# Kernel tuning notes

Measured on AMD Instinct MI355X. Metric: run time of the kernel, lower is better.

The kernel has to match this reference:

```python
import jax, jax.numpy as jnp
import numpy as np


def setup_inputs() -> dict:
    key = jax.random.key(0)
    ks = jax.random.split(key, 7)
    B, I, H, O, T = 1024, 2048, 2048, 2048, 30
    s = 1.0 / np.sqrt(H)
    return {
        "x": jax.random.normal(ks[0], (B, I), dtype=jnp.float32),
        "w_ih": jax.random.uniform(ks[1], (3 * H, I), jnp.float32, -s, s),
        "w_hh": jax.random.uniform(ks[2], (3 * H, H), jnp.float32, -s, s),
        "b_ih": jax.random.uniform(ks[3], (3 * H,), jnp.float32, -s, s),
        "b_hh": jax.random.uniform(ks[4], (3 * H,), jnp.float32, -s, s),
        "w_cls": jax.random.uniform(ks[5], (O, H), jnp.float32, -s, s),
        "b_cls": jax.random.uniform(ks[6], (O,), jnp.float32, -s, s),
        "num_timesteps": T,
    }


def reference(x, w_ih, w_hh, b_ih, b_hh, w_cls, b_cls, num_timesteps):
    # Original module never updates hidden_unit inside the loop, so every
    # timestep computes GRUCell(x, 0) -> identical output. Compute once,
    # broadcast across T (same math as the torch loop).
    # GRUCell with h=0: W_hh @ h vanishes; only bias_hh contributes.
    gi = x @ w_ih.T + b_ih                      # [B, 3H]
    i_r, i_z, i_n = jnp.split(gi, 3, axis=1)    # each [B, H]
    h_r, h_z, h_n = jnp.split(b_hh, 3)          # each [H]
    r = jax.nn.sigmoid(i_r + h_r)
    z = jax.nn.sigmoid(i_z + h_z)
    n = jnp.tanh(i_n + r * h_n)
    h_new = (1.0 - z) * n                       # + z * 0
    out = jax.nn.sigmoid(h_new @ w_cls.T + b_cls)  # [B, O]
    B, O = out.shape
    # torch stacks along dim 2 -> [B, O, T]; squeeze is a no-op for B,O,T > 1
    return jnp.broadcast_to(out[:, :, None], (B, O, num_timesteps))
```

## Files before the change

kernel.cpp:

```cpp
#include <hip/hip_runtime.h>
#include <hip/hip_bf16.h>
#include <math.h>

typedef __attribute__((ext_vector_type(8))) _Float16 f16x8;
typedef __attribute__((ext_vector_type(4))) float f32x4;

static __device__ __forceinline__ float sigmoidf_(float x) {
    return 1.0f / (1.0f + expf(-x));
}

__global__ void cvt_all(const float* __restrict__ s0, _Float16* __restrict__ d0, int n0,
                        const float* __restrict__ s1, _Float16* __restrict__ d1, int n1,
                        const float* __restrict__ s2, _Float16* __restrict__ d2, int n2,
                        int ck01, int ck2)
{
    int c = blockIdx.x * 256 + threadIdx.x;
    const float* s; _Float16* d; int ck;
    if (c < n0)            { s = s0; d = d0; ck = ck01; }
    else if (c < n0 + n1)  { c -= n0; s = s1; d = d1; ck = ck01; }
    else                   { c -= n0 + n1; if (c >= n2) return; s = s2; d = d2; ck = ck2; }
    const int row = c / ck;
    const int kc  = c - row * ck;
    const int kcs = (kc & ~7) | ((kc & 7) ^ (row & 7));
    const float* sp = s + (size_t)c * 8;
    float4 v0 = *(const float4*)sp;
    float4 v1 = *(const float4*)(sp + 4);
    f16x8 h;
    h[0] = (_Float16)v0.x; h[1] = (_Float16)v0.y;
    h[2] = (_Float16)v0.z; h[3] = (_Float16)v0.w;
    h[4] = (_Float16)v1.x; h[5] = (_Float16)v1.y;
    h[6] = (_Float16)v1.z; h[7] = (_Float16)v1.w;
    *(f16x8*)(d + (size_t)row * ((size_t)ck * 8) + (size_t)kcs * 8) = h;
}

template <int BM, int BN, int EPI>
__launch_bounds__(256, 2)
__global__ void gemm_mw(const _Float16* __restrict__ A, const _Float16* __restrict__ Bw,
                        const float* __restrict__ bias, void* __restrict__ Cv,
                        int N, int K)
{
    constexpr int BK = 64;
    constexpr int WM = BM / 2, WN = BN / 2;
    constexpr int MR = WM / 16, NR = WN / 16;

    __shared__ _Float16 As[BM * BK];
    __shared__ _Float16 Bs[BN * BK];

    const int tid  = threadIdx.x;
    const int lane = tid & 63;
    const int wid  = tid >> 6;
    const int wr   = wid >> 1;
    const int wc   = wid & 1;
    const int brow = blockIdx.y * BM;
    const int bcol = blockIdx.x * BN;
    const int lr   = lane & 15;
    const int kb   = lane >> 4;

    const _Float16* ap = A  + (size_t)(brow + (tid >> 3)) * K + (tid & 7) * 8;
    const _Float16* bp = Bw + (size_t)(bcol + (tid >> 3)) * K + (tid & 7) * 8;

    f32x4 acc[MR][NR] = {};

    for (int k0 = 0; k0 < K; k0 += BK) {
        __syncthreads();
#pragma unroll
        for (int c0 = 0; c0 < BM * 8; c0 += 256)
            __builtin_amdgcn_global_load_lds(
                (const __attribute__((address_space(1))) void*)(ap + k0 + (size_t)(c0 >> 3) * K),
                (__attribute__((address_space(3))) void*)&As[(c0 + tid) * 8],
                16, 0, 0);
#pragma unroll
        for (int c0 = 0; c0 < BN * 8; c0 += 256)
            __builtin_amdgcn_global_load_lds(
                (const __attribute__((address_space(1))) void*)(bp + k0 + (size_t)(c0 >> 3) * K),
                (__attribute__((address_space(3))) void*)&Bs[(c0 + tid) * 8],
                16, 0, 0);
        __syncthreads();

#pragma unroll
        for (int ks = 0; ks < 2; ++ks) {
            f16x8 af[MR], bf[NR];
#pragma unroll
            for (int m = 0; m < MR; ++m) {
                const int row = wr * WM + m * 16 + lr;
                af[m] = *(const f16x8*)&As[row * BK + ((ks * 4 + kb) ^ (row & 7)) * 8];
            }
#pragma unroll
            for (int n = 0; n < NR; ++n) {
                const int row = wc * WN + n * 16 + lr;
                bf[n] = *(const f16x8*)&Bs[row * BK + ((ks * 4 + kb) ^ (row & 7)) * 8];
            }
#pragma unroll
            for (int n = 0; n < NR; ++n)
#pragma unroll
                for (int m = 0; m < MR; ++m)
                    acc[m][n] = __builtin_amdgcn_mfma_f32_16x16x32_f16(af[m], bf[n], acc[m][n], 0, 0, 0);
        }
    }

#pragma unroll
    for (int m = 0; m < MR; ++m) {
        const int r0 = brow + wr * WM + m * 16 + kb * 4;
#pragma unroll
        for (int n = 0; n < NR; ++n) {
            const int col = bcol + wc * WN + n * 16 + lr;
            const float bv = bias[col];
#pragma unroll
            for (int j = 0; j < 4; ++j) {
                const float v = acc[m][n][j] + bv;
                if (EPI == 0)
                    ((_Float16*)Cv)[(size_t)(r0 + j) * N + col] = (_Float16)v;
                else
                    ((float*)Cv)[(size_t)(r0 + j) * N + col] = sigmoidf_(v);
            }
        }
    }
}

__global__ void gate_swz(const _Float16* __restrict__ gi, const float* __restrict__ b_hh,
                         _Float16* __restrict__ hn, int B, int H)
{
    const int ch = H >> 3;
    const int c = blockIdx.x * 256 + threadIdx.x;
    if (c >= B * ch) return;
    const int b  = c / ch;
    const int hc = c - b * ch;
    const int h0 = hc * 8;
    const _Float16* g = gi + (size_t)b * 3 * H + h0;
    f16x8 ir = *(const f16x8*)g;
    f16x8 iz = *(const f16x8*)(g + H);
    f16x8 in = *(const f16x8*)(g + 2 * H);
    float hr[8], hz[8], hnn[8];
    *(float4*)&hr[0]  = *(const float4*)(b_hh + h0);
    *(float4*)&hr[4]  = *(const float4*)(b_hh + h0 + 4);
    *(float4*)&hz[0]  = *(const float4*)(b_hh + H + h0);
    *(float4*)&hz[4]  = *(const float4*)(b_hh + H + h0 + 4);
    *(float4*)&hnn[0] = *(const float4*)(b_hh + 2 * H + h0);
    *(float4*)&hnn[4] = *(const float4*)(b_hh + 2 * H + h0 + 4);
    f16x8 o;
#pragma unroll
    for (int q = 0; q < 8; ++q) {
        const float r = sigmoidf_((float)ir[q] + hr[q]);
        const float z = sigmoidf_((float)iz[q] + hz[q]);
        o[q] = (_Float16)((1.0f - z) * tanhf((float)in[q] + r * hnn[q]));
    }
    const int hcs = (hc & ~7) | ((hc & 7) ^ (b & 7));
    *(f16x8*)(hn + (size_t)b * H + (size_t)hcs * 8) = o;
}

__global__ void bcast_kernel(const float* __restrict__ res,
                             float* __restrict__ out, int BO, int T)
{
    const int bo0 = blockIdx.x * 256;
    if (T & 1) {
        float* op = out + (size_t)bo0 * T;
        const int n = 256 * T;
        for (int j = threadIdx.x; j < n; j += blockDim.x)
            op[j] = res[bo0 + j / T];
    } else {
        const int half = T >> 1;
        float2* o2 = (float2*)(out + (size_t)bo0 * T);
        const int n2 = 256 * half;
        for (int j = threadIdx.x; j < n2; j += blockDim.x) {
            const float v = res[bo0 + j / half];
            o2[j] = make_float2(v, v);
        }
    }
}

extern "C" void kernel_launch(void* const* d_in, const int* in_sizes, int n_in,
                              void* d_out, int out_size, void* d_ws, size_t ws_size,
                              hipStream_t stream)
{
    const float* x     = (const float*)d_in[0];
    const float* w_ih  = (const float*)d_in[1];
    const float* b_ih  = (const float*)d_in[3];
    const float* b_hh  = (const float*)d_in[4];
    const float* w_cls = (const float*)d_in[5];
    const float* b_cls = (const float*)d_in[6];

    const int H3 = in_sizes[3];
    const int H  = H3 / 3;
    const int I  = in_sizes[1] / H3;
    const int B  = in_sizes[0] / I;
    const int O  = in_sizes[6];
    const int T  = out_size / (B * O);

    _Float16* x16    = (_Float16*)d_ws;
    _Float16* wcls16 = x16 + (size_t)B * I;
    _Float16* hn16   = wcls16 + (size_t)O * H;
    float*    res    = (float*)(hn16 + (size_t)B * H);

    _Float16* wih16 = (_Float16*)d_out;
    _Float16* gi16  = wih16 + (size_t)H3 * I;

    dim3 blk(256);

    {
        const int n0 = B * I / 8, n1 = H3 * I / 8, n2 = O * H / 8;
        const int tot = n0 + n1 + n2;
        cvt_all<<<(tot + 255) / 256, blk, 0, stream>>>(x, x16, n0, w_ih, wih16, n1,
                                                       w_cls, wcls16, n2, I / 8, H / 8);
    }

    gemm_mw<128, 96, 0><<<dim3(H3 / 96, B / 128), blk, 0, stream>>>(
        x16, wih16, b_ih, gi16, H3, I);

    gate_swz<<<(B * H / 8 + 255) / 256, blk, 0, stream>>>(gi16, b_hh, hn16, B, H);

    gemm_mw<64, 64, 1><<<dim3(O / 64, B / 64), blk, 0, stream>>>(
        hn16, wcls16, b_cls, res, O, H);

    bcast_kernel<<<(B * O) / 256, blk, 0, stream>>>(res, (float*)d_out, B * O, T);
}
```

Before: 411.0 us.

## Fuse GRU gate into first GEMM and broadcast into classifier GEMM with double buffering

The first GEMM now tiles over the three gate slices of one hidden range, so the r/z/n gate math runs in its epilogue and the f16 gi intermediate plus the separate gate kernel go away. The classifier GEMM stages sigmoid outputs in shared memory and writes the T-fold broadcast output directly, removing the res buffer and the broadcast kernel. Both GEMMs switch to double-buffered LDS with global_load_lds prefetch of the next K tile, at the cost of more shared memory per block and possibly lower occupancy. The broadcast write pattern from each block is less contiguous than the old flat broadcast kernel.

```diff
diff --git a/kernel.cpp b/kernel.cpp
--- a/kernel.cpp
+++ b/kernel.cpp
@@ -8,6 +8,10 @@
 static __device__ __forceinline__ float sigmoidf_(float x) {
     return 1.0f / (1.0f + expf(-x));
 }
+
+#define GLL(src, dst) __builtin_amdgcn_global_load_lds(                         \
+        (const __attribute__((address_space(1))) void*)(src),                   \
+        (__attribute__((address_space(3))) void*)(dst), 16, 0, 0)
 
 __global__ void cvt_all(const float* __restrict__ s0, _Float16* __restrict__ d0, int n0,
                         const float* __restrict__ s1, _Float16* __restrict__ d1, int n1,
@@ -33,62 +37,166 @@
     *(f16x8*)(d + (size_t)row * ((size_t)ck * 8) + (size_t)kcs * 8) = h;
 }
 
-template <int BM, int BN, int EPI>
 __launch_bounds__(256, 2)
-__global__ void gemm_mw(const _Float16* __restrict__ A, const _Float16* __restrict__ Bw,
-                        const float* __restrict__ bias, void* __restrict__ Cv,
-                        int N, int K)
-{
-    constexpr int BK = 64;
-    constexpr int WM = BM / 2, WN = BN / 2;
-    constexpr int MR = WM / 16, NR = WN / 16;
-
-    __shared__ _Float16 As[BM * BK];
-    __shared__ _Float16 Bs[BN * BK];
+__global__ void gemm1_gate(const _Float16* __restrict__ A,
+                           const _Float16* __restrict__ W,
+                           const float* __restrict__ b_ih,
+                           const float* __restrict__ b_hh,
+                           _Float16* __restrict__ hn,
+                           int H, int I)
+{
+    constexpr int BM = 128, BNH = 32, BN = 96, BK = 64;
+    constexpr int MR = 2, NR = 6;
+
+    __shared__ _Float16 As[2][BM * BK];
+    __shared__ _Float16 Bs[2][BN * BK];
+
+    const int tid  = threadIdx.x;
+    const int lane = tid & 63;
+    const int wid  = tid >> 6;
+    const int lr   = lane & 15;
+    const int kb   = lane >> 4;
+    const int brow = blockIdx.y * BM;
+    const int h0   = blockIdx.x * BNH;
+
+    const _Float16* asrc[4];
+#pragma unroll
+    for (int i = 0; i < 4; ++i) {
+        const int c = i * 256 + tid;
+        asrc[i] = A + (size_t)(brow + (c >> 3)) * I + (c & 7) * 8;
+    }
+    const _Float16* bsrc[3];
+#pragma unroll
+    for (int i = 0; i < 3; ++i) {
+        const int c = i * 256 + tid;
+        const int r = c >> 3, grp = r >> 5, hr = r & 31;
+        bsrc[i] = W + (size_t)(grp * H + h0 + hr) * I + (c & 7) * 8;
+    }
+
+    f32x4 acc[MR][NR] = {};
+
+    auto stage = [&](int buf, int kt) {
+#pragma unroll
+        for (int i = 0; i < 4; ++i)
+            GLL(asrc[i] + (size_t)kt * BK, &As[buf][(i * 256 + tid) * 8]);
+#pragma unroll
+        for (int i = 0; i < 3; ++i)
+            GLL(bsrc[i] + (size_t)kt * BK, &Bs[buf][(i * 256 + tid) * 8]);
+    };
+    auto compute = [&](int buf) {
+#pragma unroll
+        for (int ks = 0; ks < 2; ++ks) {
+            f16x8 af[MR], bf[NR];
+#pragma unroll
+            for (int m = 0; m < MR; ++m) {
+                const int row = wid * 32 + m * 16 + lr;
+                af[m] = *(const f16x8*)&As[buf][row * BK + ((ks * 4 + kb) ^ (row & 7)) * 8];
+            }
+#pragma unroll
+            for (int n = 0; n < NR; ++n) {
+                const int row = n * 16 + lr;
+                bf[n] = *(const f16x8*)&Bs[buf][row * BK + ((ks * 4 + kb) ^ (row & 7)) * 8];
+            }
+#pragma unroll
+            for (int n = 0; n < NR; ++n)
+#pragma unroll
+                for (int m = 0; m < MR; ++m)
+                    acc[m][n] = __builtin_amdgcn_mfma_f32_16x16x32_f16(af[m], bf[n], acc[m][n], 0, 0, 0);
+        }
+    };
+
+    const int nt = I / BK;
+    stage(0, 0);
+    __syncthreads();
+    int cur = 0;
+    for (int t = 0; t < nt - 1; ++t) {
+        stage(cur ^ 1, t + 1);
+        compute(cur);
+        __syncthreads();
+        cur ^= 1;
+    }
+    compute(cur);
+
+#pragma unroll
+    for (int q = 0; q < 2; ++q) {
+        const int h  = h0 + q * 16 + lr;
+        const float br_ = b_ih[h]         + b_hh[h];
+        const float bz_ = b_ih[H + h]     + b_hh[H + h];
+        const float bn_ = b_ih[2 * H + h];
+        const float hnb = b_hh[2 * H + h];
+        const int hc  = h >> 3;
+        const int hlo = h & 7;
+#pragma unroll
+        for (int m = 0; m < MR; ++m) {
+            const int r0 = brow + wid * 32 + m * 16 + kb * 4;
+#pragma unroll
+            for (int j = 0; j < 4; ++j) {
+                const int b = r0 + j;
+                const float rr = sigmoidf_(acc[m][q][j]     + br_);
+                const float zz = sigmoidf_(acc[m][q + 2][j] + bz_);
+                const float hv = (1.0f - zz) * tanhf(acc[m][q + 4][j] + bn_ + rr * hnb);
+                const int hcs = (hc & ~7) | ((hc & 7) ^ (b & 7));
+                hn[(size_t)b * H + hcs * 8 + hlo] = (_Float16)hv;
+            }
+        }
+    }
+}
+
+__launch_bounds__(256, 2)
+__global__ void gemm2_bcast(const _Float16* __restrict__ A,
+                            const _Float16* __restrict__ Bw,
+                            const float* __restrict__ bias,
+                            float* __restrict__ out,
+                            int O, int K, int T)
+{
+    constexpr int BT = 64, BK = 64;
+    constexpr int MR = 2, NR = 2;
+
+    __shared__ _Float16 As[2][BT * BK];
+    __shared__ _Float16 Bs[2][BT * BK];
+    __shared__ float resS[64][65];
 
     const int tid  = threadIdx.x;
     const int lane = tid & 63;
     const int wid  = tid >> 6;
     const int wr   = wid >> 1;
     const int wc   = wid & 1;
-    const int brow = blockIdx.y * BM;
-    const int bcol = blockIdx.x * BN;
     const int lr   = lane & 15;
     const int kb   = lane >> 4;
-
-    const _Float16* ap = A  + (size_t)(brow + (tid >> 3)) * K + (tid & 7) * 8;
-    const _Float16* bp = Bw + (size_t)(bcol + (tid >> 3)) * K + (tid & 7) * 8;
+    const int brow = blockIdx.y * BT;
+    const int bcol = blockIdx.x * BT;
+
+    const _Float16* asrc[2];
+    const _Float16* bsrc[2];
+#pragma unroll
+    for (int i = 0; i < 2; ++i) {
+        const int c = i * 256 + tid;
+        asrc[i] = A  + (size_t)(brow + (c >> 3)) * K + (c & 7) * 8;
+        bsrc[i] = Bw + (size_t)(bcol + (c >> 3)) * K + (c & 7) * 8;
+    }
 
     f32x4 acc[MR][NR] = {};
 
-    for (int k0 = 0; k0 < K; k0 += BK) {
-        __syncthreads();
-#pragma unroll
-        for (int c0 = 0; c0 < BM * 8; c0 += 256)
-            __builtin_amdgcn_global_load_lds(
-                (const __attribute__((address_space(1))) void*)(ap + k0 + (size_t)(c0 >> 3) * K),
-                (__attribute__((address_space(3))) void*)&As[(c0 + tid) * 8],
-                16, 0, 0);
-#pragma unroll
-        for (int c0 = 0; c0 < BN * 8; c0 += 256)
-            __builtin_amdgcn_global_load_lds(
-                (const __attribute__((address_space(1))) void*)(bp + k0 + (size_t)(c0 >> 3) * K),
-                (__attribute__((address_space(3))) void*)&Bs[(c0 + tid) * 8],
-                16, 0, 0);
-        __syncthreads();
-
+    auto stage = [&](int buf, int kt) {
+#pragma unroll
+        for (int i = 0; i < 2; ++i) {
+            GLL(asrc[i] + (size_t)kt * BK, &As[buf][(i * 256 + tid) * 8]);
+            GLL(bsrc[i] + (size_t)kt * BK, &Bs[buf][(i * 256 + tid) * 8]);
+        }
+    };
+    auto compute = [&](int buf) {
 #pragma unroll
         for (int ks = 0; ks < 2; ++ks) {
             f16x8 af[MR], bf[NR];
 #pragma unroll
             for (int m = 0; m < MR; ++m) {
-                const int row = wr * WM + m * 16 + lr;
-                af[m] = *(const f16x8*)&As[row * BK + ((ks * 4 + kb) ^ (row & 7)) * 8];
+                const int row = wr * 32 + m * 16 + lr;
+                af[m] = *(const f16x8*)&As[buf][row * BK + ((ks * 4 + kb) ^ (row & 7)) * 8];
             }
 #pragma unroll
             for (int n = 0; n < NR; ++n) {
-                const int row = wc * WN + n * 16 + lr;
-                bf[n] = *(const f16x8*)&Bs[row * BK + ((ks * 4 + kb) ^ (row & 7)) * 8];
+                const int row = wc * 32 + n * 16 + lr;
+                bf[n] = *(const f16x8*)&Bs[buf][row * BK + ((ks * 4 + kb) ^ (row & 7)) * 8];
             }
 #pragma unroll
             for (int n = 0; n < NR; ++n)
@@ -96,74 +204,52 @@
                 for (int m = 0; m < MR; ++m)
                     acc[m][n] = __builtin_amdgcn_mfma_f32_16x16x32_f16(af[m], bf[n], acc[m][n], 0, 0, 0);
         }
-    }
+    };
+
+    const int nt = K / BK;
+    stage(0, 0);
+    __syncthreads();
+    int cur = 0;
+    for (int t = 0; t < nt - 1; ++t) {
+        stage(cur ^ 1, t + 1);
+        compute(cur);
+        __syncthreads();
+        cur ^= 1;
+    }
+    compute(cur);
 
 #pragma unroll
     for (int m = 0; m < MR; ++m) {
-        const int r0 = brow + wr * WM + m * 16 + kb * 4;
+        const int rl = wr * 32 + m * 16 + kb * 4;
 #pragma unroll
         for (int n = 0; n < NR; ++n) {
-            const int col = bcol + wc * WN + n * 16 + lr;
-            const float bv = bias[col];
-#pragma unroll
-            for (int j = 0; j < 4; ++j) {
-                const float v = acc[m][n][j] + bv;
-                if (EPI == 0)
-                    ((_Float16*)Cv)[(size_t)(r0 + j) * N + col] = (_Float16)v;
-                else
-                    ((float*)Cv)[(size_t)(r0 + j) * N + col] = sigmoidf_(v);
-            }
-        }
-    }
-}
-
-__global__ void gate_swz(const _Float16* __restrict__ gi, const float* __restrict__ b_hh,
-                         _Float16* __restrict__ hn, int B, int H)
-{
-    const int ch = H >> 3;
-    const int c = blockIdx.x * 256 + threadIdx.x;
-    if (c >= B * ch) return;
-    const int b  = c / ch;
-    const int hc = c - b * ch;
-    const int h0 = hc * 8;
-    const _Float16* g = gi + (size_t)b * 3 * H + h0;
-    f16x8 ir = *(const f16x8*)g;
-    f16x8 iz = *(const f16x8*)(g + H);
-    f16x8 in = *(const f16x8*)(g + 2 * H);
-    float hr[8], hz[8], hnn[8];
-    *(float4*)&hr[0]  = *(const float4*)(b_hh + h0);
-    *(float4*)&hr[4]  = *(const float4*)(b_hh + h0 + 4);
-    *(float4*)&hz[0]  = *(const float4*)(b_hh + H + h0);
-    *(float4*)&hz[4]  = *(const float4*)(b_hh + H + h0 + 4);
-    *(float4*)&hnn[0] = *(const float4*)(b_hh + 2 * H + h0);
-    *(float4*)&hnn[4] = *(const float4*)(b_hh + 2 * H + h0 + 4);
-    f16x8 o;
-#pragma unroll
-    for (int q = 0; q < 8; ++q) {
-        const float r = sigmoidf_((float)ir[q] + hr[q]);
-        const float z = sigmoidf_((float)iz[q] + hz[q]);
-        o[q] = (_Float16)((1.0f - z) * tanhf((float)in[q] + r * hnn[q]));
-    }
-    const int hcs = (hc & ~7) | ((hc & 7) ^ (b & 7));
-    *(f16x8*)(hn + (size_t)b * H + (size_t)hcs * 8) = o;
-}
-
-__global__ void bcast_kernel(const float* __restrict__ res,
-                             float* __restrict__ out, int BO, int T)
-{
-    const int bo0 = blockIdx.x * 256;
-    if (T & 1) {
-        float* op = out + (size_t)bo0 * T;
-        const int n = 256 * T;
-        for (int j = threadIdx.x; j < n; j += blockDim.x)
-            op[j] = res[bo0 + j / T];
+            const int cl = wc * 32 + n * 16 + lr;
+            const float bv = bias[bcol + cl];
+#pragma unroll
+            for (int j = 0; j < 4; ++j)
+                resS[rl + j][cl] = sigmoidf_(acc[m][n][j] + bv);
+        }
+    }
+    __syncthreads();
+
+    if (!(T & 1)) {
+        const int ppr = 32 * T;
+        const int hT  = T >> 1;
+        for (int j = tid; j < 64 * ppr; j += 256) {
+            const int rl  = j / ppr;
+            const int rem = j - rl * ppr;
+            const int ol  = rem / hT;
+            const float v = resS[rl][ol];
+            float2* p = (float2*)out + ((size_t)(brow + rl) * O + bcol) * hT + rem;
+            *p = make_float2(v, v);
+        }
     } else {
-        const int half = T >> 1;
-        float2* o2 = (float2*)(out + (size_t)bo0 * T);
-        const int n2 = 256 * half;
-        for (int j = threadIdx.x; j < n2; j += blockDim.x) {
-            const float v = res[bo0 + j / half];
-            o2[j] = make_float2(v, v);
+        const int ppr = 64 * T;
+        for (int j = tid; j < 64 * ppr; j += 256) {
+            const int rl  = j / ppr;
+            const int rem = j - rl * ppr;
+            const int ol  = rem / T;
+            out[((size_t)(brow + rl) * O + bcol) * T + rem] = resS[rl][ol];
         }
     }
 }
@@ -189,10 +275,8 @@
     _Float16* x16    = (_Float16*)d_ws;
     _Float16* wcls16 = x16 + (size_t)B * I;
     _Float16* hn16   = wcls16 + (size_t)O * H;
-    float*    res    = (float*)(hn16 + (size_t)B * H);
 
     _Float16* wih16 = (_Float16*)d_out;
-    _Float16* gi16  = wih16 + (size_t)H3 * I;
 
     dim3 blk(256);
 
@@ -203,13 +287,9 @@
                                                        w_cls, wcls16, n2, I / 8, H / 8);
     }
 
-    gemm_mw<128, 96, 0><<<dim3(H3 / 96, B / 128), blk, 0, stream>>>(
-        x16, wih16, b_ih, gi16, H3, I);
-
-    gate_swz<<<(B * H / 8 + 255) / 256, blk, 0, stream>>>(gi16, b_hh, hn16, B, H);
-
-    gemm_mw<64, 64, 1><<<dim3(O / 64, B / 64), blk, 0, stream>>>(
-        hn16, wcls16, b_cls, res, O, H);
-
-    bcast_kernel<<<(B * O) / 256, blk, 0, stream>>>(res, (float*)d_out, B * O, T);
-}
+    gemm1_gate<<<dim3(H / 32, B / 128), blk, 0, stream>>>(
+        x16, wih16, b_ih, b_hh, hn16, H, I);
+
+    gemm2_bcast<<<dim3(O / 64, B / 64), blk, 0, stream>>>(
+        hn16, wcls16, b_cls, (float*)d_out, O, H, T);
+}
```

Result: no change. 416.0 us (+1.2%).
